# Optimization experiments

Measured on AMD Instinct MI355X. Metric: run time of the kernel, lower is better.

The kernel has to match this reference:

```python
import jax, jax.numpy as jnp
import numpy as np

D_MODEL = 2048
NHEAD = 16
HEAD_DIM = D_MODEL // NHEAD
LN_EPS = 1e-5


def setup_inputs() -> dict:
    key = jax.random.key(0)
    ks = jax.random.split(key, 5)
    B, S, D = 4, 2048, D_MODEL
    scale = 1.0 / np.sqrt(D)
    return {
        "x": jax.random.normal(ks[0], (B, S, D), dtype=jnp.float32),
        "Wq": jax.random.normal(ks[1], (D, D), dtype=jnp.float32) * scale,
        "Wv": jax.random.normal(ks[2], (D, D), dtype=jnp.float32) * scale,
        "Wg": jax.random.normal(ks[3], (D, D), dtype=jnp.float32) * scale,
        "Wo": jax.random.normal(ks[4], (D, D), dtype=jnp.float32) * scale,
        "beta": jnp.full((NHEAD,), -0.2, dtype=jnp.float32),
        "ln_w": jnp.ones((D,), dtype=jnp.float32),
        "ln_b": jnp.zeros((D,), dtype=jnp.float32),
    }


def reference(x, Wq, Wv, Wg, Wo, beta, ln_w, ln_b):
    B, S, D = x.shape
    H, hd = NHEAD, HEAD_DIM
    # projections (nn.Linear: y = x @ W.T)
    q = (x @ Wq.T).reshape(B, S, H, hd)
    v = (x @ Wv.T).reshape(B, S, H, hd)
    lam = jax.nn.sigmoid(beta)[None, :, None]  # [1,H,1]
    # decay recurrence: state_t = lam * state_{t-1} + v_t  (state_0 = v_0)
    def step(carry, vt):
        carry = lam * carry + vt
        return carry, carry
    v_t = jnp.swapaxes(v, 0, 1)  # [S,B,H,hd]
    _, st = jax.lax.scan(step, jnp.zeros((B, H, hd), dtype=v.dtype), v_t)
    state = jnp.swapaxes(st, 0, 1)  # [B,S,H,hd]
    y = (q * state).reshape(B, S, D)
    # LayerNorm over last dim
    mu = jnp.mean(y, axis=-1, keepdims=True)
    var = jnp.mean(jnp.square(y - mu), axis=-1, keepdims=True)
    y = (y - mu) * jax.lax.rsqrt(var + LN_EPS) * ln_w + ln_b
    # SiLU gate
    gate = jax.nn.silu(x @ Wg.T)
    y = y * gate
    return y @ Wo.T
```

## Files before the change

kernel.cpp:

```cpp
#include <hip/hip_runtime.h>
#include <cstdint>
#include <cstddef>

#define D_MODEL 2048
#define NHEAD 16
#define HEAD_DIM 128
#define BATCH 4
#define SEQ 2048
#define MROWS (BATCH * SEQ)
#define LN_EPS 1e-5f

typedef __bf16 bf16x8 __attribute__((ext_vector_type(8)));
typedef float f32x4 __attribute__((ext_vector_type(4)));
typedef unsigned short u16x8 __attribute__((ext_vector_type(8)));

static __device__ __forceinline__ unsigned short f2bf(float f) {
    unsigned u = __float_as_uint(f);
    u += 0x7FFFu + ((u >> 16) & 1u);
    return (unsigned short)(u >> 16);
}
static __device__ __forceinline__ float bf2f(unsigned short h) {
    return __uint_as_float(((unsigned)h) << 16);
}

typedef __attribute__((address_space(1))) const unsigned int gu32_t;
typedef __attribute__((address_space(3))) unsigned int lu32_t;
static __device__ __forceinline__ void load_lds16(const unsigned short* g,
                                                  unsigned short* l) {
    __builtin_amdgcn_global_load_lds((gu32_t*)g, (lu32_t*)l, 16, 0, 0);
}

__global__ void cast_kernel(const float* __restrict__ in,
                            unsigned short* __restrict__ out, int n) {
    int i = (blockIdx.x * blockDim.x + threadIdx.x) * 4;
    if (i >= n) return;
    float4 f = *(const float4*)(in + i);
    ushort4 o;
    o.x = f2bf(f.x); o.y = f2bf(f.y); o.z = f2bf(f.z); o.w = f2bf(f.w);
    *(ushort4*)(out + i) = o;
}

__global__ void cast4_kernel(const float* __restrict__ w0, const float* __restrict__ w1,
                             const float* __restrict__ w2, const float* __restrict__ w3,
                             unsigned short* __restrict__ out) {
    const long SZW = (long)D_MODEL * D_MODEL;
    int m = blockIdx.x >> 12;
    long i = ((long)(blockIdx.x & 4095) * 256 + threadIdx.x) * 4;
    const float* w = (m == 0) ? w0 : (m == 1) ? w1 : (m == 2) ? w2 : w3;
    float4 f = *(const float4*)(w + i);
    ushort4 o;
    o.x = f2bf(f.x); o.y = f2bf(f.y); o.z = f2bf(f.z); o.w = f2bf(f.w);
    *(ushort4*)(out + m * SZW + i) = o;
}

#define BAR() asm volatile("s_barrier" ::: "memory")

template<int OUT_BF16>
__global__ __launch_bounds__(512, 2) void gemm256(const unsigned short* __restrict__ A,
                                                  const unsigned short* __restrict__ Bbase,
                                                  void* __restrict__ Cv,
                                                  int M, int N, int K, int ntiles)
{
    __shared__ __align__(16) unsigned short As[2][16384];
    __shared__ __align__(16) unsigned short Bs[2][16384];
    const int tid  = threadIdx.x;
    const int wave = tid >> 6, lane = tid & 63;
    const int r = lane & 15, q4 = lane >> 4;
    const int wr = wave >> 2, wc = wave & 3;
    const int mat = blockIdx.x / ntiles;
    const int xt  = blockIdx.x % ntiles;
    const int bm  = (int)blockIdx.y << 8;
    const int bn  = xt << 8;
    const unsigned short* B = Bbase + (long)mat * N * (long)K;

    int offA[2][2], offB[2][2];
#pragma unroll
    for (int h = 0; h < 2; ++h)
#pragma unroll
        for (int i = 0; i < 2; ++i) {
            int off  = h * 16384 + i * 8192 + wave * 1024 + (lane << 4);
            int row  = off >> 7;
            int colb = (off & 127) ^ ((row & 7) << 4);
            offA[h][i] = (bm + row) * (K * 2) + colb;
            offB[h][i] = (bn + row) * (K * 2) + colb;
        }
    const int xr  = (r & 7) << 4;
    const int cs0 = ((q4 * 16) ^ xr) >> 1;
    const int cs1 = ((64 + q4 * 16) ^ xr) >> 1;

    f32x4 acc[8][4];
#pragma unroll
    for (int i = 0; i < 8; ++i)
#pragma unroll
        for (int j = 0; j < 4; ++j) acc[i][j] = (f32x4){0.f, 0.f, 0.f, 0.f};

    const char* Ac = (const char*)A;
    const char* Bc = (const char*)B;
    auto stA = [&](int buf, int h, int kt) {
        load_lds16((const unsigned short*)(Ac + offA[h][0] + kt * 128),
                   &As[buf][h * 8192 + wave * 512]);
        load_lds16((const unsigned short*)(Ac + offA[h][1] + kt * 128),
                   &As[buf][h * 8192 + 4096 + wave * 512]);
    };
    auto stB = [&](int buf, int h, int kt) {
        load_lds16((const unsigned short*)(Bc + offB[h][0] + kt * 128),
                   &Bs[buf][h * 8192 + wave * 512]);
        load_lds16((const unsigned short*)(Bc + offB[h][1] + kt * 128),
                   &Bs[buf][h * 8192 + 4096 + wave * 512]);
    };
    auto rdA = [&](const unsigned short* Ab, int p, bf16x8 dst[2][2]) {
#pragma unroll
        for (int ii = 0; ii < 2; ++ii) {
            dst[ii][0] = *(const bf16x8*)&Ab[(wr * 128 + (2 * p + ii) * 16 + r) * 64 + cs0];
            dst[ii][1] = *(const bf16x8*)&Ab[(wr * 128 + (2 * p + ii) * 16 + r) * 64 + cs1];
        }
    };

    const int nt = K >> 6;
    stA(0, 0, 0); stA(0, 1, 0);
    stB(0, 0, 0); stB(0, 1, 0);
    stB(1, 0, 1); stB(1, 1, 1);
    asm volatile("s_waitcnt vmcnt(4)" ::: "memory");
    BAR();

    for (int t = 0; t < nt; ++t) {
        const int c = t & 1;
        const unsigned short* Ab = As[c];
        const unsigned short* Bb = Bs[c];
        bf16x8 afA[2][2], afB[2][2];
        bf16x8 bfr[4][2];

#pragma unroll
        for (int j = 0; j < 4; ++j) {
            bfr[j][0] = *(const bf16x8*)&Bb[(wc * 64 + j * 16 + r) * 64 + cs0];
            bfr[j][1] = *(const bf16x8*)&Bb[(wc * 64 + j * 16 + r) * 64 + cs1];
        }
        rdA(Ab, 0, afA);
        rdA(Ab, 1, afB);
        if (t + 1 < nt) stA(c ^ 1, 0, t + 1);
        __builtin_amdgcn_s_setprio(1);
#pragma unroll
        for (int ks = 0; ks < 2; ++ks)
#pragma unroll
            for (int ii = 0; ii < 2; ++ii)
#pragma unroll
                for (int j = 0; j < 4; ++j)
                    acc[0 + ii][j] = __builtin_amdgcn_mfma_f32_16x16x32_bf16(
                        afA[ii][ks], bfr[j][ks], acc[0 + ii][j], 0, 0, 0);
        __builtin_amdgcn_s_setprio(0);
        BAR();

        rdA(Ab, 2, afA);
        if (t + 1 < nt) stA(c ^ 1, 1, t + 1);
        __builtin_amdgcn_s_setprio(1);
#pragma unroll
        for (int ks = 0; ks < 2; ++ks)
#pragma unroll
            for (int ii = 0; ii < 2; ++ii)
#pragma unroll
                for (int j = 0; j < 4; ++j)
                    acc[2 + ii][j] = __builtin_amdgcn_mfma_f32_16x16x32_bf16(
                        afB[ii][ks], bfr[j][ks], acc[2 + ii][j], 0, 0, 0);
        __builtin_amdgcn_s_setprio(0);
        BAR();

        rdA(Ab, 3, afB);
        if (t + 2 < nt) stB(c, 0, t + 2);
        __builtin_amdgcn_s_setprio(1);
#pragma unroll
        for (int ks = 0; ks < 2; ++ks)
#pragma unroll
            for (int ii = 0; ii < 2; ++ii)
#pragma unroll
                for (int j = 0; j < 4; ++j)
                    acc[4 + ii][j] = __builtin_amdgcn_mfma_f32_16x16x32_bf16(
                        afA[ii][ks], bfr[j][ks], acc[4 + ii][j], 0, 0, 0);
        __builtin_amdgcn_s_setprio(0);
        BAR();

        if (t + 2 < nt) stB(c, 1, t + 2);
        __builtin_amdgcn_s_setprio(1);
#pragma unroll
        for (int ks = 0; ks < 2; ++ks)
#pragma unroll
            for (int ii = 0; ii < 2; ++ii)
#pragma unroll
                for (int j = 0; j < 4; ++j)
                    acc[6 + ii][j] = __builtin_amdgcn_mfma_f32_16x16x32_bf16(
                        afB[ii][ks], bfr[j][ks], acc[6 + ii][j], 0, 0, 0);
        __builtin_amdgcn_s_setprio(0);
        asm volatile("s_waitcnt vmcnt(4)" ::: "memory");
        BAR();
    }

    const long cmat = (long)mat * M * (long)N;
#pragma unroll
    for (int i = 0; i < 8; ++i) {
#pragma unroll
        for (int j = 0; j < 4; ++j) {
            long row = bm + wr * 128 + i * 16 + q4 * 4;
            long col = bn + wc * 64 + j * 16 + r;
#pragma unroll
            for (int e = 0; e < 4; ++e) {
                float val = acc[i][j][e];
                if (OUT_BF16)
                    ((unsigned short*)Cv)[cmat + (row + e) * (long)N + col] = f2bf(val);
                else
                    ((float*)Cv)[cmat + (row + e) * (long)N + col] = val;
            }
        }
    }
}

#define FCHUNK 32
#define FWARM 64
__global__ __launch_bounds__(256) void retn_ln_kernel(
    const unsigned short* __restrict__ qb,
    const unsigned short* __restrict__ vb,
    const unsigned short* __restrict__ gb,
    const float* __restrict__ beta,
    const float* __restrict__ ln_w,
    const float* __restrict__ ln_b,
    unsigned short* __restrict__ y2)
{
    __shared__ __align__(16) unsigned short y_lds[FCHUNK][D_MODEL];
    __shared__ float ssum[4][8][4], ssq[4][8][4];
    const int tid  = threadIdx.x;
    const int wid  = tid >> 6, lane = tid & 63;
    const int b    = blockIdx.x >> 6;
    const int c    = blockIdx.x & 63;
    const int s0   = c * FCHUNK;
    const int e0   = tid * 8;
    const int h    = tid >> 4;
    const float lam = 1.f / (1.f + expf(-beta[h]));
    const long rowbase = (long)b * SEQ;

    float st[8];
#pragma unroll
    for (int i = 0; i < 8; ++i) st[i] = 0.f;

    int sw = s0 - FWARM; if (sw < 0) sw = 0;
    for (int s = sw; s < s0; s += 8) {
        u16x8 vv[8];
#pragma unroll
        for (int k = 0; k < 8; ++k)
            vv[k] = *(const u16x8*)&vb[(rowbase + s + k) * D_MODEL + e0];
#pragma unroll
        for (int k = 0; k < 8; ++k)
#pragma unroll
            for (int i = 0; i < 8; ++i) st[i] = lam * st[i] + bf2f(vv[k][i]);
    }
    for (int ls = 0; ls < FCHUNK; ls += 8) {
        u16x8 vv[8], qq[8];
#pragma unroll
        for (int k = 0; k < 8; ++k)
            vv[k] = *(const u16x8*)&vb[(rowbase + s0 + ls + k) * D_MODEL + e0];
#pragma unroll
        for (int k = 0; k < 8; ++k)
            qq[k] = *(const u16x8*)&qb[(rowbase + s0 + ls + k) * D_MODEL + e0];
#pragma unroll
        for (int k = 0; k < 8; ++k) {
            u16x8 o;
#pragma unroll
            for (int i = 0; i < 8; ++i) {
                st[i] = lam * st[i] + bf2f(vv[k][i]);
                o[i]  = f2bf(bf2f(qq[k][i]) * st[i]);
            }
            *(u16x8*)&y_lds[ls + k][e0] = o;
        }
    }
    __syncthreads();

    float lw[8], lb[8];
    {
        float4 a0 = *(const float4*)&ln_w[e0];
        float4 a1 = *(const float4*)&ln_w[e0 + 4];
        float4 b0 = *(const float4*)&ln_b[e0];
        float4 b1 = *(const float4*)&ln_b[e0 + 4];
        lw[0]=a0.x; lw[1]=a0.y; lw[2]=a0.z; lw[3]=a0.w;
        lw[4]=a1.x; lw[5]=a1.y; lw[6]=a1.z; lw[7]=a1.w;
        lb[0]=b0.x; lb[1]=b0.y; lb[2]=b0.z; lb[3]=b0.w;
        lb[4]=b1.x; lb[5]=b1.y; lb[6]=b1.z; lb[7]=b1.w;
    }

    for (int g = 0; g < 4; ++g) {
        u16x8 gv[8], yv[8];
#pragma unroll
        for (int tt = 0; tt < 8; ++tt)
            gv[tt] = *(const u16x8*)&gb[(rowbase + s0 + g * 8 + tt) * D_MODEL + e0];
        float psum[8], psq[8];
#pragma unroll
        for (int tt = 0; tt < 8; ++tt) {
            yv[tt] = *(const u16x8*)&y_lds[g * 8 + tt][e0];
            float su = 0.f, sq = 0.f;
#pragma unroll
            for (int i = 0; i < 8; ++i) { float f = bf2f(yv[tt][i]); su += f; sq += f * f; }
            psum[tt] = su; psq[tt] = sq;
        }
#pragma unroll
        for (int off = 32; off > 0; off >>= 1)
#pragma unroll
            for (int tt = 0; tt < 8; ++tt) {
                psum[tt] += __shfl_down(psum[tt], off);
                psq[tt]  += __shfl_down(psq[tt],  off);
            }
        if (lane == 0)
#pragma unroll
            for (int tt = 0; tt < 8; ++tt) { ssum[g][tt][wid] = psum[tt]; ssq[g][tt][wid] = psq[tt]; }
        __syncthreads();
#pragma unroll
        for (int tt = 0; tt < 8; ++tt) {
            float sum = ssum[g][tt][0] + ssum[g][tt][1] + ssum[g][tt][2] + ssum[g][tt][3];
            float sq  = ssq[g][tt][0]  + ssq[g][tt][1]  + ssq[g][tt][2]  + ssq[g][tt][3];
            float mu  = sum * (1.f / D_MODEL);
            float var = sq * (1.f / D_MODEL) - mu * mu;
            float rs  = rsqrtf(var + LN_EPS);
            u16x8 ov;
#pragma unroll
            for (int i = 0; i < 8; ++i) {
                float gf   = bf2f(gv[tt][i]);
                float gate = gf / (1.f + expf(-gf));
                float yvf  = (bf2f(yv[tt][i]) - mu) * rs * lw[i] + lb[i];
                ov[i] = f2bf(yvf * gate);
            }
            *(u16x8*)&y2[(rowbase + s0 + g * 8 + tt) * D_MODEL + e0] = ov;
        }
    }
}

extern "C" void kernel_launch(void* const* d_in, const int* in_sizes, int n_in,
                              void* d_out, int out_size, void* d_ws, size_t ws_size,
                              hipStream_t stream)
{
    (void)in_sizes; (void)n_in; (void)out_size; (void)ws_size;
    const float* x    = (const float*)d_in[0];
    const float* Wq   = (const float*)d_in[1];
    const float* Wv   = (const float*)d_in[2];
    const float* Wg   = (const float*)d_in[3];
    const float* Wo   = (const float*)d_in[4];
    const float* beta = (const float*)d_in[5];
    const float* lnw  = (const float*)d_in[6];
    const float* lnb  = (const float*)d_in[7];

    const long SZX = (long)MROWS * D_MODEL;
    const long SZW = (long)D_MODEL * D_MODEL;

    unsigned short* ws  = (unsigned short*)d_ws;
    unsigned short* xb  = ws;
    unsigned short* wqb = xb + SZX;
    unsigned short* wvb = wqb + SZW;
    unsigned short* wgb = wvb + SZW;
    unsigned short* wob = wgb + SZW;
    unsigned short* qb  = wob + SZW;
    unsigned short* vb  = qb + SZX;
    unsigned short* gb  = vb + SZX;

    cast_kernel<<<(int)(SZX / 1024), 256, 0, stream>>>(x, xb, (int)SZX);
    cast4_kernel<<<4 * (int)(SZW / 1024), 256, 0, stream>>>(Wq, Wv, Wg, Wo, wqb);

    dim3 gridQVG(3 * (D_MODEL / 256), MROWS / 256);
    gemm256<1><<<gridQVG, 512, 0, stream>>>(xb, wqb, qb,
                                            MROWS, D_MODEL, D_MODEL, D_MODEL / 256);

    retn_ln_kernel<<<BATCH * (SEQ / FCHUNK), 256, 0, stream>>>(qb, vb, gb,
                                                               beta, lnw, lnb, xb);

    dim3 gridO(D_MODEL / 256, MROWS / 256);
    gemm256<0><<<gridO, 512, 0, stream>>>(xb, wob, d_out,
                                          MROWS, D_MODEL, D_MODEL, D_MODEL / 256);
}
```

Baseline: 463.3 us.

## Prefetch A tiles two k-steps ahead alongside B in GEMM pipeline

Restructures the GEMM main loop so the A tile, like B, is prefetched two iterations ahead into the double buffer, instead of one step ahead inside the current iteration. A fragments are now read per phase into four separate register sets, and explicit lgkmcnt waits with sched barriers are added before the barriers that precede overwriting the LDS regions. The goal is deeper global-load latency hiding for A. In exchange it uses more registers for fragments, which could hurt occupancy at the 2-block launch bound, and adds extra LDS waits.

```diff
diff --git a/kernel.cpp b/kernel.cpp
--- a/kernel.cpp
+++ b/kernel.cpp
@@ -54,6 +54,8 @@
 }
 
 #define BAR() asm volatile("s_barrier" ::: "memory")
+#define LGKM0() do { asm volatile("s_waitcnt lgkmcnt(0)" ::: "memory"); \
+                     __builtin_amdgcn_sched_barrier(0); } while (0)
 
 template<int OUT_BF16>
 __global__ __launch_bounds__(512, 2) void gemm256(const unsigned short* __restrict__ A,
@@ -119,15 +121,21 @@
     const int nt = K >> 6;
     stA(0, 0, 0); stA(0, 1, 0);
     stB(0, 0, 0); stB(0, 1, 0);
-    stB(1, 0, 1); stB(1, 1, 1);
-    asm volatile("s_waitcnt vmcnt(4)" ::: "memory");
+    if (nt > 1) {
+        stA(1, 0, 1); stA(1, 1, 1);
+        stB(1, 0, 1); stB(1, 1, 1);
+        asm volatile("s_waitcnt vmcnt(8)" ::: "memory");
+    } else {
+        asm volatile("s_waitcnt vmcnt(0)" ::: "memory");
+    }
     BAR();
 
     for (int t = 0; t < nt; ++t) {
         const int c = t & 1;
         const unsigned short* Ab = As[c];
         const unsigned short* Bb = Bs[c];
-        bf16x8 afA[2][2], afB[2][2];
+        const bool pf = (t + 2 < nt);
+        bf16x8 af0[2][2], af1[2][2], af2[2][2], af3[2][2];
         bf16x8 bfr[4][2];
 
 #pragma unroll
@@ -135,9 +143,7 @@
             bfr[j][0] = *(const bf16x8*)&Bb[(wc * 64 + j * 16 + r) * 64 + cs0];
             bfr[j][1] = *(const bf16x8*)&Bb[(wc * 64 + j * 16 + r) * 64 + cs1];
         }
-        rdA(Ab, 0, afA);
-        rdA(Ab, 1, afB);
-        if (t + 1 < nt) stA(c ^ 1, 0, t + 1);
+        rdA(Ab, 0, af0);
         __builtin_amdgcn_s_setprio(1);
 #pragma unroll
         for (int ks = 0; ks < 2; ++ks)
@@ -146,26 +152,28 @@
 #pragma unroll
                 for (int j = 0; j < 4; ++j)
                     acc[0 + ii][j] = __builtin_amdgcn_mfma_f32_16x16x32_bf16(
-                        afA[ii][ks], bfr[j][ks], acc[0 + ii][j], 0, 0, 0);
+                        af0[ii][ks], bfr[j][ks], acc[0 + ii][j], 0, 0, 0);
+        __builtin_amdgcn_s_setprio(0);
+        LGKM0();
+        BAR();
+
+        rdA(Ab, 1, af1);
+        rdA(Ab, 2, af2);
+        if (pf) stB(c, 0, t + 2);
+        __builtin_amdgcn_s_setprio(1);
+#pragma unroll
+        for (int ks = 0; ks < 2; ++ks)
+#pragma unroll
+            for (int ii = 0; ii < 2; ++ii)
+#pragma unroll
+                for (int j = 0; j < 4; ++j)
+                    acc[2 + ii][j] = __builtin_amdgcn_mfma_f32_16x16x32_bf16(
+                        af1[ii][ks], bfr[j][ks], acc[2 + ii][j], 0, 0, 0);
         __builtin_amdgcn_s_setprio(0);
         BAR();
 
-        rdA(Ab, 2, afA);
-        if (t + 1 < nt) stA(c ^ 1, 1, t + 1);
-        __builtin_amdgcn_s_setprio(1);
-#pragma unroll
-        for (int ks = 0; ks < 2; ++ks)
-#pragma unroll
-            for (int ii = 0; ii < 2; ++ii)
-#pragma unroll
-                for (int j = 0; j < 4; ++j)
-                    acc[2 + ii][j] = __builtin_amdgcn_mfma_f32_16x16x32_bf16(
-                        afB[ii][ks], bfr[j][ks], acc[2 + ii][j], 0, 0, 0);
-        __builtin_amdgcn_s_setprio(0);
-        BAR();
-
-        rdA(Ab, 3, afB);
-        if (t + 2 < nt) stB(c, 0, t + 2);
+        rdA(Ab, 3, af3);
+        if (pf) stB(c, 1, t + 2);
         __builtin_amdgcn_s_setprio(1);
 #pragma unroll
         for (int ks = 0; ks < 2; ++ks)
@@ -174,11 +182,12 @@
 #pragma unroll
                 for (int j = 0; j < 4; ++j)
                     acc[4 + ii][j] = __builtin_amdgcn_mfma_f32_16x16x32_bf16(
-                        afA[ii][ks], bfr[j][ks], acc[4 + ii][j], 0, 0, 0);
+                        af2[ii][ks], bfr[j][ks], acc[4 + ii][j], 0, 0, 0);
         __builtin_amdgcn_s_setprio(0);
+        LGKM0();
         BAR();
 
-        if (t + 2 < nt) stB(c, 1, t + 2);
+        if (pf) { stA(c, 0, t + 2); stA(c, 1, t + 2); }
         __builtin_amdgcn_s_setprio(1);
 #pragma unroll
         for (int ks = 0; ks < 2; ++ks)
@@ -187,9 +196,12 @@
 #pragma unroll
                 for (int j = 0; j < 4; ++j)
                     acc[6 + ii][j] = __builtin_amdgcn_mfma_f32_16x16x32_bf16(
-                        afB[ii][ks], bfr[j][ks], acc[6 + ii][j], 0, 0, 0);
+                        af3[ii][ks], bfr[j][ks], acc[6 + ii][j], 0, 0, 0);
         __builtin_amdgcn_s_setprio(0);
-        asm volatile("s_waitcnt vmcnt(4)" ::: "memory");
+        if (pf)
+            asm volatile("s_waitcnt vmcnt(8)" ::: "memory");
+        else
+            asm volatile("s_waitcnt vmcnt(0)" ::: "memory");
         BAR();
     }
 
```

Result: no change. 457.9 us (-1.2%).

## Restructure 256x256 GEMM mainloop into quadrant-based ping-pong with finer LDS staging

Applied to the files above, without the earlier changes.

Each wave's output sub-tile is remapped so it covers four 64x32 quadrants spread across the block tile, instead of one contiguous 128x64 strip. A and B halves are read from LDS per quadrant and reused across two MFMA phases each. Global-to-LDS loads for the next tile are interleaved at half-tile granularity, A is prefetched earlier, and explicit lgkmcnt waits plus sched barriers are placed mid-phase. The aim is better overlap of LDS reads and global loads with MFMA, and fewer LDS reads per phase. In exchange it adds barriers and holds more fragment registers live.

```diff
diff --git a/kernel.cpp b/kernel.cpp
--- a/kernel.cpp
+++ b/kernel.cpp
@@ -54,6 +54,9 @@
 }
 
 #define BAR() asm volatile("s_barrier" ::: "memory")
+#define MIDSYNC() do { BAR(); \
+    asm volatile("s_waitcnt lgkmcnt(0)" ::: "memory"); \
+    __builtin_amdgcn_sched_barrier(0); } while (0)
 
 template<int OUT_BF16>
 __global__ __launch_bounds__(512, 2) void gemm256(const unsigned short* __restrict__ A,
@@ -108,98 +111,113 @@
         load_lds16((const unsigned short*)(Bc + offB[h][1] + kt * 128),
                    &Bs[buf][h * 8192 + 4096 + wave * 512]);
     };
-    auto rdA = [&](const unsigned short* Ab, int p, bf16x8 dst[2][2]) {
-#pragma unroll
-        for (int ii = 0; ii < 2; ++ii) {
-            dst[ii][0] = *(const bf16x8*)&Ab[(wr * 128 + (2 * p + ii) * 16 + r) * 64 + cs0];
-            dst[ii][1] = *(const bf16x8*)&Ab[(wr * 128 + (2 * p + ii) * 16 + r) * 64 + cs1];
+    auto rdAh = [&](const unsigned short* Ab, int ih, bf16x8 dst[4][2]) {
+#pragma unroll
+        for (int m = 0; m < 4; ++m) {
+            int rowh = wr * 64 + m * 16 + r;
+            dst[m][0] = *(const bf16x8*)&Ab[ih * 8192 + rowh * 64 + cs0];
+            dst[m][1] = *(const bf16x8*)&Ab[ih * 8192 + rowh * 64 + cs1];
+        }
+    };
+    auto rdBh = [&](const unsigned short* Bb, int jh, bf16x8 dst[2][2]) {
+#pragma unroll
+        for (int n = 0; n < 2; ++n) {
+            int rowh = wc * 32 + n * 16 + r;
+            dst[n][0] = *(const bf16x8*)&Bb[jh * 8192 + rowh * 64 + cs0];
+            dst[n][1] = *(const bf16x8*)&Bb[jh * 8192 + rowh * 64 + cs1];
         }
     };
 
     const int nt = K >> 6;
     stA(0, 0, 0); stA(0, 1, 0);
     stB(0, 0, 0); stB(0, 1, 0);
-    stB(1, 0, 1); stB(1, 1, 1);
-    asm volatile("s_waitcnt vmcnt(4)" ::: "memory");
+    if (nt > 1) {
+        stB(1, 0, 1); stA(1, 0, 1);
+        asm volatile("s_waitcnt vmcnt(4)" ::: "memory");
+    } else {
+        asm volatile("s_waitcnt vmcnt(0)" ::: "memory");
+    }
     BAR();
 
-    for (int t = 0; t < nt; ++t) {
-        const int c = t & 1;
-        const unsigned short* Ab = As[c];
-        const unsigned short* Bb = Bs[c];
-        bf16x8 afA[2][2], afB[2][2];
-        bf16x8 bfr[4][2];
-
+    for (int X = 0; X < nt; ++X) {
+        const int x = X & 1;
+        const unsigned short* Ab = As[x];
+        const unsigned short* Bb = Bs[x];
+        const bool p1 = (X + 1 < nt), p2 = (X + 2 < nt);
+        bf16x8 a0[4][2], a1[4][2], b0[2][2], b1[2][2];
+
+        rdAh(Ab, 0, a0);
+        rdBh(Bb, 0, b0);
+        if (p1) stA(x ^ 1, 1, X + 1);
+        MIDSYNC();
+        __builtin_amdgcn_s_setprio(1);
+#pragma unroll
+        for (int ks = 0; ks < 2; ++ks)
+#pragma unroll
+            for (int m = 0; m < 4; ++m)
+#pragma unroll
+                for (int n = 0; n < 2; ++n)
+                    acc[m][n] = __builtin_amdgcn_mfma_f32_16x16x32_bf16(
+                        a0[m][ks], b0[n][ks], acc[m][n], 0, 0, 0);
+        __builtin_amdgcn_s_setprio(0);
+        BAR();
+
+        rdAh(Ab, 1, a1);
+        if (p1) stB(x ^ 1, 1, X + 1);
+        MIDSYNC();
+        __builtin_amdgcn_s_setprio(1);
+#pragma unroll
+        for (int ks = 0; ks < 2; ++ks)
+#pragma unroll
+            for (int m = 0; m < 4; ++m)
+#pragma unroll
+                for (int n = 0; n < 2; ++n)
+                    acc[4 + m][n] = __builtin_amdgcn_mfma_f32_16x16x32_bf16(
+                        a1[m][ks], b0[n][ks], acc[4 + m][n], 0, 0, 0);
+        __builtin_amdgcn_s_setprio(0);
+        BAR();
+
+        rdBh(Bb, 1, b1);
+        if (p2) stB(x, 0, X + 2);
+        MIDSYNC();
+        __builtin_amdgcn_s_setprio(1);
+#pragma unroll
+        for (int ks = 0; ks < 2; ++ks)
+#pragma unroll
+            for (int m = 0; m < 4; ++m)
+#pragma unroll
+                for (int n = 0; n < 2; ++n)
+                    acc[m][2 + n] = __builtin_amdgcn_mfma_f32_16x16x32_bf16(
+                        a0[m][ks], b1[n][ks], acc[m][2 + n], 0, 0, 0);
+        __builtin_amdgcn_s_setprio(0);
+        BAR();
+
+        if (p2) stA(x, 0, X + 2);
+        BAR();
+        __builtin_amdgcn_s_setprio(1);
+#pragma unroll
+        for (int ks = 0; ks < 2; ++ks)
+#pragma unroll
+            for (int m = 0; m < 4; ++m)
+#pragma unroll
+                for (int n = 0; n < 2; ++n)
+                    acc[4 + m][2 + n] = __builtin_amdgcn_mfma_f32_16x16x32_bf16(
+                        a1[m][ks], b1[n][ks], acc[4 + m][2 + n], 0, 0, 0);
+        __builtin_amdgcn_s_setprio(0);
+        if (p2)
+            asm volatile("s_waitcnt vmcnt(4)" ::: "memory");
+        else
+            asm volatile("s_waitcnt vmcnt(0)" ::: "memory");
+        BAR();
+    }
+
+    const long cmat = (long)mat * M * (long)N;
+#pragma unroll
+    for (int i = 0; i < 8; ++i) {
 #pragma unroll
         for (int j = 0; j < 4; ++j) {
-            bfr[j][0] = *(const bf16x8*)&Bb[(wc * 64 + j * 16 + r) * 64 + cs0];
-            bfr[j][1] = *(const bf16x8*)&Bb[(wc * 64 + j * 16 + r) * 64 + cs1];
-        }
-        rdA(Ab, 0, afA);
-        rdA(Ab, 1, afB);
-        if (t + 1 < nt) stA(c ^ 1, 0, t + 1);
-        __builtin_amdgcn_s_setprio(1);
-#pragma unroll
-        for (int ks = 0; ks < 2; ++ks)
-#pragma unroll
-            for (int ii = 0; ii < 2; ++ii)
-#pragma unroll
-                for (int j = 0; j < 4; ++j)
-                    acc[0 + ii][j] = __builtin_amdgcn_mfma_f32_16x16x32_bf16(
-                        afA[ii][ks], bfr[j][ks], acc[0 + ii][j], 0, 0, 0);
-        __builtin_amdgcn_s_setprio(0);
-        BAR();
-
-        rdA(Ab, 2, afA);
-        if (t + 1 < nt) stA(c ^ 1, 1, t + 1);
-        __builtin_amdgcn_s_setprio(1);
-#pragma unroll
-        for (int ks = 0; ks < 2; ++ks)
-#pragma unroll
-            for (int ii = 0; ii < 2; ++ii)
-#pragma unroll
-                for (int j = 0; j < 4; ++j)
-                    acc[2 + ii][j] = __builtin_amdgcn_mfma_f32_16x16x32_bf16(
-                        afB[ii][ks], bfr[j][ks], acc[2 + ii][j], 0, 0, 0);
-        __builtin_amdgcn_s_setprio(0);
-        BAR();
-
-        rdA(Ab, 3, afB);
-        if (t + 2 < nt) stB(c, 0, t + 2);
-        __builtin_amdgcn_s_setprio(1);
-#pragma unroll
-        for (int ks = 0; ks < 2; ++ks)
-#pragma unroll
-            for (int ii = 0; ii < 2; ++ii)
-#pragma unroll
-                for (int j = 0; j < 4; ++j)
-                    acc[4 + ii][j] = __builtin_amdgcn_mfma_f32_16x16x32_bf16(
-                        afA[ii][ks], bfr[j][ks], acc[4 + ii][j], 0, 0, 0);
-        __builtin_amdgcn_s_setprio(0);
-        BAR();
-
-        if (t + 2 < nt) stB(c, 1, t + 2);
-        __builtin_amdgcn_s_setprio(1);
-#pragma unroll
-        for (int ks = 0; ks < 2; ++ks)
-#pragma unroll
-            for (int ii = 0; ii < 2; ++ii)
-#pragma unroll
-                for (int j = 0; j < 4; ++j)
-                    acc[6 + ii][j] = __builtin_amdgcn_mfma_f32_16x16x32_bf16(
-                        afB[ii][ks], bfr[j][ks], acc[6 + ii][j], 0, 0, 0);
-        __builtin_amdgcn_s_setprio(0);
-        asm volatile("s_waitcnt vmcnt(4)" ::: "memory");
-        BAR();
-    }
-
-    const long cmat = (long)mat * M * (long)N;
-#pragma unroll
-    for (int i = 0; i < 8; ++i) {
-#pragma unroll
-        for (int j = 0; j < 4; ++j) {
-            long row = bm + wr * 128 + i * 16 + q4 * 4;
-            long col = bn + wc * 64 + j * 16 + r;
+            long row = bm + (i >> 2) * 128 + wr * 64 + (i & 3) * 16 + q4 * 4;
+            long col = bn + (j >> 1) * 128 + wc * 32 + (j & 1) * 16 + r;
 #pragma unroll
             for (int e = 0; e < 4; ++e) {
                 float val = acc[i][j][e];
```

Result: no change. 460.8 us (-0.5%).
